# Optimization experiments

Measured on AMD Instinct MI355X. Metric: run time of the kernel, lower is better.

## Reference

```python
import jax, jax.numpy as jnp
import numpy as np

OUTPUT_DIM = 1024
D_K = 1024  # Lt feature dim
D_Q = 1024  # rnn_ht feature dim
SCALE = 1.0 / np.sqrt(64.0)  # hardcoded 64**0.5 in original, NOT sqrt(output_dim)


def setup_inputs() -> dict:
    key = jax.random.key(0)
    k1, k2, k3, k4 = jax.random.split(key, 4)
    B, Sq, Sk = 8, 2048, 2048
    Lt = jax.random.normal(k1, (B, Sk, D_K), dtype=jnp.float32)
    rnn_ht = jax.random.normal(k2, (B, Sq, D_Q), dtype=jnp.float32)
    # 'uniform' keras initializer: U(-0.05, 0.05)
    kernel = jax.random.uniform(k3, (2, D_K, OUTPUT_DIM), dtype=jnp.float32, minval=-0.05, maxval=0.05)
    W = jax.random.uniform(k4, (D_Q, OUTPUT_DIM), dtype=jnp.float32, minval=-0.05, maxval=0.05)
    return {"Lt": Lt, "rnn_ht": rnn_ht, "kernel": kernel, "W": W}


def reference(Lt, rnn_ht, kernel, W):
    WQ = jnp.einsum('bsd,de->bse', rnn_ht, W)          # [B, Sq, E]
    WK = jnp.einsum('bsd,de->bse', Lt, kernel[0])      # [B, Sk, E]
    WV = jnp.einsum('bsd,de->bse', Lt, kernel[1])      # [B, Sk, E]
    QK = jnp.einsum('bqe,bke->bqk', WQ, WK) * SCALE    # [B, Sq, Sk]
    weights = jax.nn.softmax(QK, axis=-1)
    context_vector = jnp.einsum('bqk,bke->bqe', weights, WV)  # [B, Sq, E]
    return (context_vector, weights)
```

## Files before the change

kernel.cpp:

```cpp
#include <hip/hip_runtime.h>


typedef __bf16 bf16x8 __attribute__((ext_vector_type(8)));
typedef __bf16 bf16x4 __attribute__((ext_vector_type(4)));
typedef float  f32x4  __attribute__((ext_vector_type(4)));

__device__ __forceinline__ void gload_lds16(const void* g, void* l) {
  __builtin_amdgcn_global_load_lds(
      (__attribute__((address_space(1))) void*)(g),
      (__attribute__((address_space(3))) void*)(uintptr_t)(l),
      16, 0, 0);
}

__device__ __forceinline__ void ldfrag4(bf16x8 (&f)[4], const __bf16* reg_,
                                        int rbase, int fm, int gq) {
#pragma unroll
  for (int i = 0; i < 4; ++i) {
    const int r = rbase + i * 16 + fm;
    f[i] = *(const bf16x8*)(reg_ + r * 32 + ((gq ^ ((r >> 1) & 3)) << 3));
  }
}

__device__ __forceinline__ void stage16(const __bf16* src, __bf16* dst,
                                        size_t rowstride, int wave, int lane) {
#pragma unroll
  for (int i = 0; i < 2; ++i) {
    const int chunk = wave * 2 + i;
    const int row = chunk * 16 + (lane >> 2);
    const int gg = (lane & 3) ^ ((row >> 1) & 3);
    gload_lds16(src + (size_t)row * rowstride + (gg << 3), dst + chunk * 512);
  }
}

template <int MH>
__device__ __forceinline__ void mfma16(f32x4 (&acc)[8][4], const bf16x8 (&a)[4],
                                       const bf16x8 (&b)[4]) {
#pragma unroll
  for (int mi = 0; mi < 4; ++mi)
#pragma unroll
    for (int nj = 0; nj < 4; ++nj)
      acc[MH * 4 + mi][nj] = __builtin_amdgcn_mfma_f32_16x16x32_bf16(
          a[mi], b[nj], acc[MH * 4 + mi][nj], 0, 0, 0);
}

#define PHASE_MID()                       \
  __builtin_amdgcn_sched_barrier(0);      \
  __builtin_amdgcn_s_barrier();           \
  __builtin_amdgcn_s_setprio(1)

#define PHASE_END()                       \
  __builtin_amdgcn_s_setprio(0);          \
  __builtin_amdgcn_sched_barrier(0);      \
  __builtin_amdgcn_s_barrier()

template <bool OUTBF16>
__device__ __forceinline__ void tile_gemm(
    const __bf16* __restrict__ Aa, const __bf16* __restrict__ Ba,
    void* __restrict__ Cp, size_t cbase, int N, int K, float scale,
    __bf16* lds, int wave, int lane, int wm, int wn, int fm, int gq) {
  __bf16* const As_ = lds;
  __bf16* const Bs_ = lds + 32768;
#define AREG(p, h) (As_ + (p) * 16384 + (h) * 8192)
#define BREG(p, h) (Bs_ + (p) * 16384 + (h) * 8192)

  f32x4 acc[8][4] = {};
  bf16x8 a[4], b[4];

  stage16(Ba + 0,  BREG(0, 0), K, wave, lane);
  stage16(Aa + 0,  AREG(0, 0), K, wave, lane);
  stage16(Ba + 32, BREG(0, 1), K, wave, lane);
  stage16(Aa + 32, AREG(0, 1), K, wave, lane);
  asm volatile("s_waitcnt vmcnt(4)" ::: "memory");
  stage16(Ba + 64, BREG(1, 0), K, wave, lane);
  stage16(Aa + 64, AREG(1, 0), K, wave, lane);
  stage16(Ba + 96, BREG(1, 1), K, wave, lane);
  asm volatile("s_waitcnt vmcnt(6)" ::: "memory");
  __builtin_amdgcn_s_barrier();

  const int niter = K >> 7;
  for (int it = 0; it < niter; ++it) {
    const int kt = it << 7;
    const bool s2 = (kt + 128) < K;

    ldfrag4(a, AREG(0, 0), wm, fm, gq);
    ldfrag4(b, BREG(0, 0), wn, fm, gq);
    stage16(Aa + kt + 96, AREG(1, 1), K, wave, lane);
    PHASE_MID();
    mfma16<0>(acc, a, b);
    PHASE_END();

    ldfrag4(a, AREG(0, 0), wm + 64, fm, gq);
    if (s2) stage16(Ba + kt + 128, BREG(0, 0), K, wave, lane);
    PHASE_MID();
    mfma16<1>(acc, a, b);
    PHASE_END();

    ldfrag4(a, AREG(0, 1), wm, fm, gq);
    ldfrag4(b, BREG(0, 1), wn, fm, gq);
    if (s2) stage16(Aa + kt + 128, AREG(0, 0), K, wave, lane);
    PHASE_MID();
    mfma16<0>(acc, a, b);
    PHASE_END();

    ldfrag4(a, AREG(0, 1), wm + 64, fm, gq);
    if (s2) stage16(Ba + kt + 160, BREG(0, 1), K, wave, lane);
    PHASE_MID();
    mfma16<1>(acc, a, b);
    __builtin_amdgcn_s_setprio(0);
    __builtin_amdgcn_sched_barrier(0);
    if (s2) { asm volatile("s_waitcnt vmcnt(6)" ::: "memory"); }
    else    { asm volatile("s_waitcnt vmcnt(0)" ::: "memory"); }
    __builtin_amdgcn_s_barrier();

    ldfrag4(a, AREG(1, 0), wm, fm, gq);
    ldfrag4(b, BREG(1, 0), wn, fm, gq);
    if (s2) stage16(Aa + kt + 160, AREG(0, 1), K, wave, lane);
    PHASE_MID();
    mfma16<0>(acc, a, b);
    PHASE_END();

    ldfrag4(a, AREG(1, 0), wm + 64, fm, gq);
    if (s2) stage16(Ba + kt + 192, BREG(1, 0), K, wave, lane);
    PHASE_MID();
    mfma16<1>(acc, a, b);
    PHASE_END();

    ldfrag4(a, AREG(1, 1), wm, fm, gq);
    ldfrag4(b, BREG(1, 1), wn, fm, gq);
    if (s2) stage16(Aa + kt + 192, AREG(1, 0), K, wave, lane);
    PHASE_MID();
    mfma16<0>(acc, a, b);
    PHASE_END();

    ldfrag4(a, AREG(1, 1), wm + 64, fm, gq);
    if (s2) stage16(Ba + kt + 224, BREG(1, 1), K, wave, lane);
    PHASE_MID();
    mfma16<1>(acc, a, b);
    __builtin_amdgcn_s_setprio(0);
    __builtin_amdgcn_sched_barrier(0);
    if (s2) { asm volatile("s_waitcnt vmcnt(6)" ::: "memory"); }
    __builtin_amdgcn_s_barrier();
  }

  const int col   = lane & 15;
  const int rquad = (lane >> 4) * 4;
#pragma unroll
  for (int mi = 0; mi < 8; ++mi) {
#pragma unroll
    for (int r = 0; r < 4; ++r) {
      const size_t roff = (size_t)(wm + mi * 16 + rquad + r) * (size_t)N;
#pragma unroll
      for (int nj = 0; nj < 4; ++nj) {
        const size_t cidx = cbase + roff + wn + nj * 16 + col;
        if constexpr (OUTBF16) {
          ((__bf16*)Cp)[cidx] = (__bf16)acc[mi][nj][r];
        } else {
          ((float*)Cp)[cidx] = acc[mi][nj][r] * scale;
        }
      }
    }
  }
#undef AREG
#undef BREG
}

__global__ __launch_bounds__(512, 2)
void proj_all(const __bf16* __restrict__ rnnb, const __bf16* __restrict__ Ltb,
              const __bf16* __restrict__ Wt, const __bf16* __restrict__ k0t,
              const __bf16* __restrict__ k1t, __bf16* __restrict__ WQ,
              __bf16* __restrict__ WK, __bf16* __restrict__ WVt) {
  __shared__ __bf16 lds[65536];
  const int tid = threadIdx.x, wave = tid >> 6, lane = tid & 63;
  const int wm = (wave >> 2) * 128, wn = (wave & 3) * 64;
  const int fm = lane & 15, gq = lane >> 4;
  const int d = blockIdx.x, x = d & 7, s = d >> 3;

  {
    const int bx = s & 3, by = x * 8 + (s >> 2);
    const size_t ao = (size_t)by * 256 * 1024;
    const size_t bo = (size_t)bx * 256 * 1024;
    const size_t cb = (size_t)by * 256 * 1024 + (size_t)bx * 256;
    tile_gemm<true>(rnnb + ao, Wt + bo, WQ, cb, 1024, 1024, 1.0f,
                    lds, wave, lane, wm, wn, fm, gq);
    tile_gemm<true>(Ltb + ao, k0t + bo, WK, cb, 1024, 1024, 1.0f,
                    lds, wave, lane, wm, wn, fm, gq);
  }
  {
    const int by = s >> 3, bx = s & 7;
    tile_gemm<true>(k1t + (size_t)by * 256 * 1024,
                    Ltb + (size_t)x * 2048 * 1024 + (size_t)bx * 256 * 1024,
                    WVt,
                    (size_t)x * 1024 * 2048 + (size_t)by * 256 * 2048 +
                        (size_t)bx * 256,
                    2048, 1024, 1.0f, lds, wave, lane, wm, wn, fm, gq);
  }
}

__global__ __launch_bounds__(512, 2)
void qk2(const __bf16* __restrict__ WQ, const __bf16* __restrict__ WK,
         float* __restrict__ wts) {
  __shared__ __bf16 lds[65536];
  const int tid = threadIdx.x, wave = tid >> 6, lane = tid & 63;
  const int wm = (wave >> 2) * 128, wn = (wave & 3) * 64;
  const int fm = lane & 15, gq = lane >> 4;
  const int d = blockIdx.x, x = d & 7, s = d >> 3;
  const int by = s >> 3, bx = s & 7;

  const __bf16* Qb = WQ + (size_t)x * 2048 * 1024;
  const __bf16* Kb = WK + (size_t)x * 2048 * 1024 + (size_t)bx * 256 * 1024;
  const size_t cb0 = (size_t)x * 2048 * 2048 + (size_t)bx * 256;

  tile_gemm<false>(Qb + (size_t)by * 256 * 1024, Kb, wts,
                   cb0 + (size_t)by * 256 * 2048, 2048, 1024, 0.125f,
                   lds, wave, lane, wm, wn, fm, gq);
  tile_gemm<false>(Qb + (size_t)(by + 4) * 256 * 1024, Kb, wts,
                   cb0 + (size_t)(by + 4) * 256 * 2048, 2048, 1024, 0.125f,
                   lds, wave, lane, wm, wn, fm, gq);
}

__global__ __launch_bounds__(512, 2)
void pv1(const __bf16* __restrict__ Pb, const __bf16* __restrict__ WVt,
         float* __restrict__ ctx) {
  __shared__ __bf16 lds[65536];
  const int tid = threadIdx.x, wave = tid >> 6, lane = tid & 63;
  const int wm = (wave >> 2) * 128, wn = (wave & 3) * 64;
  const int fm = lane & 15, gq = lane >> 4;
  const int d = blockIdx.x, x = d & 7, s = d >> 3;
  const int by = s >> 2, bx = s & 3;

  tile_gemm<false>(Pb + (size_t)x * 2048 * 2048 + (size_t)by * 256 * 2048,
                   WVt + (size_t)x * 1024 * 2048 + (size_t)bx * 256 * 2048,
                   ctx,
                   (size_t)x * 2048 * 1024 + (size_t)by * 256 * 1024 +
                       (size_t)bx * 256,
                   1024, 2048, 1.0f, lds, wave, lane, wm, wn, fm, gq);
}

__global__ __launch_bounds__(256)
void cvt_transpose(const float* __restrict__ s0, const float* __restrict__ s1,
                   const float* __restrict__ s2, __bf16* __restrict__ d0,
                   __bf16* __restrict__ d1, __bf16* __restrict__ d2) {
  const float* s = blockIdx.z == 0 ? s0 : (blockIdx.z == 1 ? s1 : s2);
  __bf16* d      = blockIdx.z == 0 ? d0 : (blockIdx.z == 1 ? d1 : d2);
  __shared__ float tile[32][33];
  const int x  = blockIdx.x * 32 + threadIdx.x;
  const int y0 = blockIdx.y * 32;
  for (int j = threadIdx.y; j < 32; j += 8)
    tile[j][threadIdx.x] = s[(size_t)(y0 + j) * 1024 + x];
  __syncthreads();
  const int x2 = y0 + threadIdx.x;
  const int y2 = blockIdx.x * 32;
  for (int j = threadIdx.y; j < 32; j += 8)
    d[(size_t)(y2 + j) * 1024 + x2] = (__bf16)tile[threadIdx.x][j];
}

__global__ __launch_bounds__(256)
void cvt_bf16(const float* __restrict__ s0, __bf16* __restrict__ d0,
              const float* __restrict__ s1, __bf16* __restrict__ d1) {
  const float* s = blockIdx.z ? s1 : s0;
  __bf16* d      = blockIdx.z ? d1 : d0;
  const size_t i = ((size_t)blockIdx.x * 256 + threadIdx.x) * 4;
  float4 f = *(const float4*)(s + i);
  bf16x4 h = {(__bf16)f.x, (__bf16)f.y, (__bf16)f.z, (__bf16)f.w};
  *(bf16x4*)(d + i) = h;
}

__global__ __launch_bounds__(256)
void softmax_rows(float* __restrict__ Wt, __bf16* __restrict__ Pb) {
  const int t = threadIdx.x;
  float* p = Wt + (size_t)blockIdx.x * 2048;
  float4 a = ((float4*)p)[t];
  float4 b = ((float4*)p)[t + 256];

  float m = fmaxf(fmaxf(fmaxf(a.x, a.y), fmaxf(a.z, a.w)),
                  fmaxf(fmaxf(b.x, b.y), fmaxf(b.z, b.w)));
#pragma unroll
  for (int off = 32; off > 0; off >>= 1) m = fmaxf(m, __shfl_xor(m, off));
  __shared__ float red[8];
  if ((t & 63) == 0) red[t >> 6] = m;
  __syncthreads();
  m = fmaxf(fmaxf(red[0], red[1]), fmaxf(red[2], red[3]));

  a.x = __expf(a.x - m); a.y = __expf(a.y - m);
  a.z = __expf(a.z - m); a.w = __expf(a.w - m);
  b.x = __expf(b.x - m); b.y = __expf(b.y - m);
  b.z = __expf(b.z - m); b.w = __expf(b.w - m);
  float s = a.x + a.y + a.z + a.w + b.x + b.y + b.z + b.w;
#pragma unroll
  for (int off = 32; off > 0; off >>= 1) s += __shfl_xor(s, off);
  if ((t & 63) == 0) red[4 + (t >> 6)] = s;
  __syncthreads();
  s = red[4] + red[5] + red[6] + red[7];

  const float inv = 1.0f / s;
  a.x *= inv; a.y *= inv; a.z *= inv; a.w *= inv;
  b.x *= inv; b.y *= inv; b.z *= inv; b.w *= inv;
  ((float4*)p)[t] = a;
  ((float4*)p)[t + 256] = b;

  __bf16* pb = Pb + (size_t)blockIdx.x * 2048;
  bf16x4 ha = {(__bf16)a.x, (__bf16)a.y, (__bf16)a.z, (__bf16)a.w};
  bf16x4 hb = {(__bf16)b.x, (__bf16)b.y, (__bf16)b.z, (__bf16)b.w};
  *(bf16x4*)(pb + (size_t)t * 4) = ha;
  *(bf16x4*)(pb + (size_t)(t + 256) * 4) = hb;
}

extern "C" void kernel_launch(void* const* d_in, const int* in_sizes, int n_in,
                              void* d_out, int out_size, void* d_ws,
                              size_t ws_size, hipStream_t stream) {
  const float* Lt  = (const float*)d_in[0];
  const float* rnn = (const float*)d_in[1];
  const float* ker = (const float*)d_in[2];
  const float* W   = (const float*)d_in[3];

  float* ctx = (float*)d_out;
  float* wts = ctx + (size_t)16777216;

  __bf16* ws   = (__bf16*)d_ws;
  __bf16* Wt   = ws;
  __bf16* k0t  = Wt + (1u << 20);
  __bf16* k1t  = k0t + (1u << 20);
  __bf16* WQ   = k1t + (1u << 20);
  __bf16* WK   = WQ + (16u << 20);
  __bf16* WVt  = WK + (16u << 20);
  __bf16* Ltb  = WVt + (16u << 20);
  __bf16* rnnb = Ltb + (16u << 20);
  __bf16* Pb = Ltb;

  cvt_transpose<<<dim3(32, 32, 3), dim3(32, 8), 0, stream>>>(
      W, ker, ker + (1u << 20), Wt, k0t, k1t);

  cvt_bf16<<<dim3(16384, 1, 2), 256, 0, stream>>>(Lt, Ltb, rnn, rnnb);

  proj_all<<<256, 512, 0, stream>>>(rnnb, Ltb, Wt, k0t, k1t, WQ, WK, WVt);

  qk2<<<256, 512, 0, stream>>>(WQ, WK, wts);

  softmax_rows<<<16384, 256, 0, stream>>>(wts, Pb);

  pv1<<<256, 512, 0, stream>>>(Pb, WVt, ctx);
}
```

Baseline: 555.9 us.

## Merge conversion kernels into one launch and drop GEMM sched barriers

Combines the weight transpose-convert and the activation bf16 conversion into a single kernel that dispatches on block index, removing one launch and the gap between them. Separately removes sched_barrier(0) calls around the MFMA phases in the tiled GEMM, letting the compiler interleave LDS loads and MFMAs across phase boundaries. Dropping the scheduling fences risks the compiler reordering in ways that hurt the hand-tuned pipeline.

```diff
diff --git a/kernel.cpp b/kernel.cpp
--- a/kernel.cpp
+++ b/kernel.cpp
@@ -44,13 +44,11 @@
 }
 
 #define PHASE_MID()                       \
-  __builtin_amdgcn_sched_barrier(0);      \
   __builtin_amdgcn_s_barrier();           \
   __builtin_amdgcn_s_setprio(1)
 
 #define PHASE_END()                       \
   __builtin_amdgcn_s_setprio(0);          \
-  __builtin_amdgcn_sched_barrier(0);      \
   __builtin_amdgcn_s_barrier()
 
 template <bool OUTBF16>
@@ -107,7 +105,6 @@
     PHASE_MID();
     mfma16<1>(acc, a, b);
     __builtin_amdgcn_s_setprio(0);
-    __builtin_amdgcn_sched_barrier(0);
     if (s2) { asm volatile("s_waitcnt vmcnt(6)" ::: "memory"); }
     else    { asm volatile("s_waitcnt vmcnt(0)" ::: "memory"); }
     __builtin_amdgcn_s_barrier();
@@ -137,7 +134,6 @@
     PHASE_MID();
     mfma16<1>(acc, a, b);
     __builtin_amdgcn_s_setprio(0);
-    __builtin_amdgcn_sched_barrier(0);
     if (s2) { asm volatile("s_waitcnt vmcnt(6)" ::: "memory"); }
     __builtin_amdgcn_s_barrier();
   }
@@ -237,32 +233,38 @@
 }
 
 __global__ __launch_bounds__(256)
-void cvt_transpose(const float* __restrict__ s0, const float* __restrict__ s1,
-                   const float* __restrict__ s2, __bf16* __restrict__ d0,
-                   __bf16* __restrict__ d1, __bf16* __restrict__ d2) {
-  const float* s = blockIdx.z == 0 ? s0 : (blockIdx.z == 1 ? s1 : s2);
-  __bf16* d      = blockIdx.z == 0 ? d0 : (blockIdx.z == 1 ? d1 : d2);
-  __shared__ float tile[32][33];
-  const int x  = blockIdx.x * 32 + threadIdx.x;
-  const int y0 = blockIdx.y * 32;
-  for (int j = threadIdx.y; j < 32; j += 8)
-    tile[j][threadIdx.x] = s[(size_t)(y0 + j) * 1024 + x];
-  __syncthreads();
-  const int x2 = y0 + threadIdx.x;
-  const int y2 = blockIdx.x * 32;
-  for (int j = threadIdx.y; j < 32; j += 8)
-    d[(size_t)(y2 + j) * 1024 + x2] = (__bf16)tile[threadIdx.x][j];
-}
-
-__global__ __launch_bounds__(256)
-void cvt_bf16(const float* __restrict__ s0, __bf16* __restrict__ d0,
-              const float* __restrict__ s1, __bf16* __restrict__ d1) {
-  const float* s = blockIdx.z ? s1 : s0;
-  __bf16* d      = blockIdx.z ? d1 : d0;
-  const size_t i = ((size_t)blockIdx.x * 256 + threadIdx.x) * 4;
-  float4 f = *(const float4*)(s + i);
-  bf16x4 h = {(__bf16)f.x, (__bf16)f.y, (__bf16)f.z, (__bf16)f.w};
-  *(bf16x4*)(d + i) = h;
+void cvt_all(const float* __restrict__ W, const float* __restrict__ ker,
+             __bf16* __restrict__ Wt, __bf16* __restrict__ k0t,
+             __bf16* __restrict__ k1t,
+             const float* __restrict__ Lt, __bf16* __restrict__ Ltb,
+             const float* __restrict__ rnn, __bf16* __restrict__ rnnb) {
+  const int d = blockIdx.x;
+  const int t = threadIdx.x;
+  if (d < 3072) {
+    const int z = d >> 10, i = d & 1023;
+    const int bx = i & 31, by = i >> 5;
+    const float* s = z == 0 ? W : (z == 1 ? ker : ker + (1u << 20));
+    __bf16* o      = z == 0 ? Wt : (z == 1 ? k0t : k1t);
+    __shared__ float tile[32][33];
+    const int tx = t & 31, ty = t >> 5;
+    const int x  = bx * 32 + tx;
+    const int y0 = by * 32;
+    for (int j = ty; j < 32; j += 8)
+      tile[j][tx] = s[(size_t)(y0 + j) * 1024 + x];
+    __syncthreads();
+    const int x2 = y0 + tx;
+    const int y2 = bx * 32;
+    for (int j = ty; j < 32; j += 8)
+      o[(size_t)(y2 + j) * 1024 + x2] = (__bf16)tile[tx][j];
+  } else {
+    const int f = d - 3072;
+    const float* s = f < 16384 ? Lt : rnn;
+    __bf16* o      = f < 16384 ? Ltb : rnnb;
+    const size_t i = ((size_t)(f & 16383) * 256 + t) * 4;
+    float4 v = *(const float4*)(s + i);
+    bf16x4 h = {(__bf16)v.x, (__bf16)v.y, (__bf16)v.z, (__bf16)v.w};
+    *(bf16x4*)(o + i) = h;
+  }
 }
 
 __global__ __launch_bounds__(256)
@@ -327,10 +329,7 @@
   __bf16* rnnb = Ltb + (16u << 20);
   __bf16* Pb = Ltb;
 
-  cvt_transpose<<<dim3(32, 32, 3), dim3(32, 8), 0, stream>>>(
-      W, ker, ker + (1u << 20), Wt, k0t, k1t);
-
-  cvt_bf16<<<dim3(16384, 1, 2), 256, 0, stream>>>(Lt, Ltb, rnn, rnnb);
+  cvt_all<<<36864, 256, 0, stream>>>(W, ker, Wt, k0t, k1t, Lt, Ltb, rnn, rnnb);
 
   proj_all<<<256, 512, 0, stream>>>(rnnb, Ltb, Wt, k0t, k1t, WQ, WK, WVt);
 
```

Result: slower. 570.2 us (+2.6%).
